# Kernel optimization log

Measured on AMD Instinct MI355X. Metric: run time of the kernel, lower is better.

The kernel has to match this reference:

```python
import jax, jax.numpy as jnp
import numpy as np

NUM_TOKENS = 8192
MODEL_DIM = 4096
NUM_EXPERTS = 64
CAPACITY_FACTOR = 1.0


def setup_inputs() -> dict:
    key = jax.random.key(0)
    k1, k2 = jax.random.split(key)
    inp = jax.random.normal(k1, (NUM_TOKENS, MODEL_DIM), dtype=jnp.float32)
    wg = jax.random.normal(k2, (NUM_EXPERTS, MODEL_DIM), dtype=jnp.float32) * (1.0 / np.sqrt(MODEL_DIM))
    return {"input": inp, "wg_weight": wg}


def reference(input, wg_weight):
    # logits = input @ wg.T  -> [T, E]
    logits = jnp.einsum('td,ed->te', input, wg_weight)
    num_tokens, num_experts = logits.shape
    capacity = int(CAPACITY_FACTOR * ((num_tokens + num_experts - 1) // num_experts))

    indices1_s = jnp.argmax(logits, axis=1)                      # [T]
    mask1 = jax.nn.one_hot(indices1_s, num_experts, dtype=logits.dtype)  # [T, E]
    gates = jax.nn.softmax(logits, axis=1)                       # [T, E]
    gates1_s = jnp.sum(gates * mask1, axis=1)                    # [T]

    # locations: position of each token within its chosen expert's queue
    # (exclusive cumsum over the one-hot mask, gathered at the chosen expert)
    locations1 = jnp.cumsum(mask1, axis=0) - 1.0                 # [T, E]
    locations1_s = jnp.sum(locations1 * mask1, axis=1).astype(jnp.int32)  # [T]

    # load-balancing aux loss (float32 branch of the original)
    me = jnp.sum(gates, axis=0)                                  # [E]
    ce = jnp.sum(mask1, axis=0)                                  # [E]
    l_aux = jnp.sum(me * ce) * (num_experts / (num_tokens * num_tokens))

    return (l_aux, indices1_s.astype(jnp.int32), locations1_s, gates1_s)
```

## Files before the change

### kernel.cpp

```cpp
#include <hip/hip_runtime.h>

namespace {
constexpr int TOK = 8192;
constexpr int DIM = 4096;
constexpr int NE  = 64;
constexpr int TB  = 128;
constexpr int KS  = 8;
constexpr int KR  = DIM / KS;
constexpr int BK  = 32;
constexpr int NT  = TOK / TB;
constexpr int NITER = KR / BK;
constexpr int LSTR = 40;
constexpr int GB  = 64;
constexpr int NCH = TOK / GB;
}

typedef _Float16 f16x8 __attribute__((ext_vector_type(8)));
typedef _Float16 f16x4 __attribute__((ext_vector_type(4)));
typedef float    f32x4 __attribute__((ext_vector_type(4)));

__global__ __launch_bounds__(256) void gemm_split(
    const float* __restrict__ A, const float* __restrict__ W,
    float* __restrict__ partial) {
  __shared__ _Float16 sm[(2 * TB + 2 * NE) * LSTR];
  _Float16* sAhi = sm;
  _Float16* sAlo = sm + TB * LSTR;
  _Float16* sWhi = sm + 2 * TB * LSTR;
  _Float16* sWlo = sm + 2 * TB * LSTR + NE * LSTR;

  const int bid  = blockIdx.x;
  const int tile = bid & (NT - 1);
  const int ks   = bid / NT;
  const int t0   = tile * TB;
  const int k0   = ks * KR;
  const int tid  = threadIdx.x;
  const int w    = tid >> 6;
  const int lane = tid & 63;
  const int col  = lane & 15;
  const int quad = lane >> 4;

  float4 ra[4], rw[2];
  {
#pragma unroll
    for (int j = 0; j < 4; ++j) {
      const int f4 = tid + 256 * j;
      const int tk = f4 >> 3, kc = (f4 & 7) * 4;
      ra[j] = *(const float4*)(A + (size_t)(t0 + tk) * DIM + k0 + kc);
    }
#pragma unroll
    for (int j = 0; j < 2; ++j) {
      const int f4 = tid + 256 * j;
      const int ee = f4 >> 3, kc = (f4 & 7) * 4;
      rw[j] = *(const float4*)(W + (size_t)ee * DIM + k0 + kc);
    }
  }

  f32x4 acc[2][4];
#pragma unroll
  for (int i = 0; i < 2; ++i)
#pragma unroll
    for (int j = 0; j < 4; ++j) acc[i][j] = (f32x4)0.0f;

  for (int it = 0; it < NITER; ++it) {
    __syncthreads();
#pragma unroll
    for (int j = 0; j < 4; ++j) {
      const int f4 = tid + 256 * j;
      const int tk = f4 >> 3, kc = (f4 & 7) * 4;
      const float4 r = ra[j];
      const _Float16 hx = (_Float16)r.x, hy = (_Float16)r.y,
                     hz = (_Float16)r.z, hw = (_Float16)r.w;
      *(f16x4*)(sAhi + tk * LSTR + kc) = (f16x4){hx, hy, hz, hw};
      *(f16x4*)(sAlo + tk * LSTR + kc) =
          (f16x4){(_Float16)(r.x - (float)hx), (_Float16)(r.y - (float)hy),
                  (_Float16)(r.z - (float)hz), (_Float16)(r.w - (float)hw)};
    }
#pragma unroll
    for (int j = 0; j < 2; ++j) {
      const int f4 = tid + 256 * j;
      const int ee = f4 >> 3, kc = (f4 & 7) * 4;
      const float4 r = rw[j];
      const _Float16 hx = (_Float16)r.x, hy = (_Float16)r.y,
                     hz = (_Float16)r.z, hw = (_Float16)r.w;
      *(f16x4*)(sWhi + ee * LSTR + kc) = (f16x4){hx, hy, hz, hw};
      *(f16x4*)(sWlo + ee * LSTR + kc) =
          (f16x4){(_Float16)(r.x - (float)hx), (_Float16)(r.y - (float)hy),
                  (_Float16)(r.z - (float)hz), (_Float16)(r.w - (float)hw)};
    }
    __syncthreads();
    if (it + 1 < NITER) {
      const int kb = k0 + (it + 1) * BK;
#pragma unroll
      for (int j = 0; j < 4; ++j) {
        const int f4 = tid + 256 * j;
        const int tk = f4 >> 3, kc = (f4 & 7) * 4;
        ra[j] = *(const float4*)(A + (size_t)(t0 + tk) * DIM + kb + kc);
      }
#pragma unroll
      for (int j = 0; j < 2; ++j) {
        const int f4 = tid + 256 * j;
        const int ee = f4 >> 3, kc = (f4 & 7) * 4;
        rw[j] = *(const float4*)(W + (size_t)ee * DIM + kb + kc);
      }
    }
    f16x8 ah[2], al[2], bh[4], bl[4];
#pragma unroll
    for (int mt = 0; mt < 2; ++mt) {
      const int r = w * 32 + mt * 16 + col;
      ah[mt] = *(const f16x8*)(sAhi + r * LSTR + quad * 8);
      al[mt] = *(const f16x8*)(sAlo + r * LSTR + quad * 8);
    }
#pragma unroll
    for (int et = 0; et < 4; ++et) {
      const int e = et * 16 + col;
      bh[et] = *(const f16x8*)(sWhi + e * LSTR + quad * 8);
      bl[et] = *(const f16x8*)(sWlo + e * LSTR + quad * 8);
    }
#pragma unroll
    for (int mt = 0; mt < 2; ++mt)
#pragma unroll
      for (int et = 0; et < 4; ++et) {
        acc[mt][et] = __builtin_amdgcn_mfma_f32_16x16x32_f16(
            ah[mt], bh[et], acc[mt][et], 0, 0, 0);
        acc[mt][et] = __builtin_amdgcn_mfma_f32_16x16x32_f16(
            ah[mt], bl[et], acc[mt][et], 0, 0, 0);
        acc[mt][et] = __builtin_amdgcn_mfma_f32_16x16x32_f16(
            al[mt], bh[et], acc[mt][et], 0, 0, 0);
      }
  }

  float* P = partial + (size_t)ks * TOK * NE;
#pragma unroll
  for (int mt = 0; mt < 2; ++mt)
#pragma unroll
    for (int et = 0; et < 4; ++et) {
      const int e = et * 16 + col;
#pragma unroll
      for (int r = 0; r < 4; ++r) {
        const int t = t0 + w * 32 + mt * 16 + quad * 4 + r;
        P[(size_t)t * NE + e] = acc[mt][et][r];
      }
    }
}

__global__ __launch_bounds__(256) void gating(
    const float* __restrict__ partial, float* __restrict__ out,
    int* __restrict__ idx_int, int* __restrict__ rankp,
    int* __restrict__ hist, float* __restrict__ me_part) {
  __shared__ float L[GB * 65];
  __shared__ float mx[GB];
  __shared__ float dninv[GB];
  __shared__ int   eid[GB];
  const int b = blockIdx.x, tid = threadIdx.x;
  const size_t base = (size_t)b * GB * NE;

#pragma unroll
  for (int j = 0; j < (GB * NE) / 256; ++j) {
    const int idx = tid + 256 * j;
    float s = 0.0f;
#pragma unroll
    for (int k = 0; k < KS; ++k)
      s += partial[(size_t)k * TOK * NE + base + idx];
    L[(idx >> 6) * 65 + (idx & 63)] = s;
  }
  __syncthreads();

  if (tid < GB) {
    const int t = tid;
    float m = -3.0e38f; int bi = 0;
    for (int e = 0; e < NE; ++e) {
      const float v = L[t * 65 + e];
      if (v > m) { m = v; bi = e; }
    }
    float s = 0.0f;
    for (int e = 0; e < NE; ++e) s += __expf(L[t * 65 + e] - m);
    const float inv = 1.0f / s;
    mx[t] = m; dninv[t] = inv; eid[t] = bi;
    const int gt = b * GB + t;
    out[1 + gt]           = (float)bi;
    out[1 + 2 * TOK + gt] = inv;
    idx_int[gt] = bi;
  }
  __syncthreads();

  if (tid < GB) {
    const int t = tid, e = eid[t];
    int r = 0;
    for (int j = 0; j < t; ++j) r += (eid[j] == e) ? 1 : 0;
    rankp[b * GB + t] = r;
    int c = 0;
    for (int t2 = 0; t2 < GB; ++t2) c += (eid[t2] == tid) ? 1 : 0;
    hist[b * NE + tid] = c;
  } else if (tid < 2 * GB) {
    const int e = tid - GB;
    float s = 0.0f;
    for (int t2 = 0; t2 < GB; ++t2)
      s += __expf(L[t2 * 65 + e] - mx[t2]) * dninv[t2];
    me_part[b * NE + e] = s;
  }
}

__global__ __launch_bounds__(256) void finalize(
    const int* __restrict__ idx_int, const int* __restrict__ rankp,
    const int* __restrict__ hist, const float* __restrict__ me_part,
    float* __restrict__ out) {
  __shared__ int   H[NCH * NE];
  __shared__ int   SEG[4 * NE];
  __shared__ float MEp[4 * NE];
  __shared__ float CE[NE];
  const int tid = threadIdx.x;
  const int e = tid & 63, seg = tid >> 6;

  for (int j = tid; j < NCH * NE; j += 256) H[j] = hist[j];
  {
    float s = 0.0f;
    for (int c = seg * 32; c < seg * 32 + 32; ++c) s += me_part[c * NE + e];
    MEp[seg * NE + e] = s;
  }
  __syncthreads();
  {
    int hs = 0;
    for (int c = seg * 32; c < seg * 32 + 32; ++c) hs += H[c * NE + e];
    SEG[seg * NE + e] = hs;
  }
  __syncthreads();
  if (tid < NE) {
    int run = 0;
    for (int s2 = 0; s2 < 4; ++s2) {
      const int v = SEG[s2 * NE + tid];
      SEG[s2 * NE + tid] = run;
      run += v;
    }
    CE[tid] = (float)run;
  }
  __syncthreads();
  {
    int run = SEG[seg * NE + e];
    for (int c = seg * 32; c < seg * 32 + 32; ++c) {
      const int v = H[c * NE + e];
      H[c * NE + e] = run;
      run += v;
    }
  }
  if (tid < 64) {
    float p = (MEp[tid] + MEp[NE + tid] + MEp[2 * NE + tid] + MEp[3 * NE + tid])
              * CE[tid];
#pragma unroll
    for (int off = 32; off > 0; off >>= 1) p += __shfl_down(p, off);
    if (tid == 0) out[0] = p * ((float)NE / ((float)TOK * (float)TOK));
  }
  __syncthreads();
#pragma unroll 4
  for (int i = tid; i < TOK; i += 256) {
    const int ex = idx_int[i];
    out[1 + TOK + i] = (float)(H[(i >> 6) * NE + ex] + rankp[i]);
  }
}

extern "C" void kernel_launch(void* const* d_in, const int* in_sizes, int n_in,
                              void* d_out, int out_size, void* d_ws, size_t ws_size,
                              hipStream_t stream) {
  const float* A = (const float*)d_in[0];
  const float* W = (const float*)d_in[1];
  float* out = (float*)d_out;
  char* ws = (char*)d_ws;

  float* partial = (float*)ws;
  const size_t poff = (size_t)KS * TOK * NE * sizeof(float);
  float* me_part = (float*)(ws + poff);
  int*  idx_int = (int*)(ws + poff + NCH * NE * sizeof(float));
  int*  rankp   = idx_int + TOK;
  int*  hist    = rankp + TOK;

  hipLaunchKernelGGL(gemm_split, dim3(NT * KS), dim3(256), 0, stream, A, W, partial);
  hipLaunchKernelGGL(gating, dim3(NCH), dim3(256), 0, stream, partial, out,
                     idx_int, rankp, hist, me_part);
  hipLaunchKernelGGL(finalize, dim3(1), dim3(256), 0, stream, idx_int, rankp,
                     hist, me_part, out);
}
```

Measured before the change: 209.6 us.

## Shrink GEMM token tile, stream A from registers, parallelize gating and finalize

The GEMM tile drops to 64 tokens per block and A fragments are loaded straight into registers in MFMA layout, so only W is split into hi/lo halves in LDS. W is double-buffered with one barrier per k-step, and launch bounds ask for higher occupancy. The gating kernel spreads max, softmax, histogram and expert-mass reductions across all 256 threads with vectorised partial loads. Finalize goes from one block to 32 blocks that each rebuild their own prefix offsets. This trades fewer barriers, less LDS traffic and more parallelism for uncoalesced-per-row A loads, twice as many GEMM blocks, and redundant histogram scans in every finalize block.

Result: no change. 209.7 us, median of 2 (+0.1%).

```diff
diff --git a/kernel.cpp b/kernel.cpp
--- a/kernel.cpp
+++ b/kernel.cpp
@@ -4,33 +4,30 @@
 constexpr int TOK = 8192;
 constexpr int DIM = 4096;
 constexpr int NE  = 64;
-constexpr int TB  = 128;
+constexpr int TB  = 64;
+constexpr int NT  = TOK / TB;
 constexpr int KS  = 8;
 constexpr int KR  = DIM / KS;
 constexpr int BK  = 32;
-constexpr int NT  = TOK / TB;
 constexpr int NITER = KR / BK;
 constexpr int LSTR = 40;
 constexpr int GB  = 64;
 constexpr int NCH = TOK / GB;
+constexpr int FB  = 32;
 }
 
 typedef _Float16 f16x8 __attribute__((ext_vector_type(8)));
 typedef _Float16 f16x4 __attribute__((ext_vector_type(4)));
 typedef float    f32x4 __attribute__((ext_vector_type(4)));
 
-__global__ __launch_bounds__(256) void gemm_split(
+__global__ __launch_bounds__(256, 4) void gemm_split(
     const float* __restrict__ A, const float* __restrict__ W,
     float* __restrict__ partial) {
-  __shared__ _Float16 sm[(2 * TB + 2 * NE) * LSTR];
-  _Float16* sAhi = sm;
-  _Float16* sAlo = sm + TB * LSTR;
-  _Float16* sWhi = sm + 2 * TB * LSTR;
-  _Float16* sWlo = sm + 2 * TB * LSTR + NE * LSTR;
+  __shared__ _Float16 sw[2][2][NE * LSTR];
 
   const int bid  = blockIdx.x;
   const int tile = bid & (NT - 1);
-  const int ks   = bid / NT;
+  const int ks   = bid >> 7;
   const int t0   = tile * TB;
   const int k0   = ks * KR;
   const int tid  = threadIdx.x;
@@ -39,108 +36,93 @@
   const int col  = lane & 15;
   const int quad = lane >> 4;
 
-  float4 ra[4], rw[2];
-  {
-#pragma unroll
-    for (int j = 0; j < 4; ++j) {
-      const int f4 = tid + 256 * j;
-      const int tk = f4 >> 3, kc = (f4 & 7) * 4;
-      ra[j] = *(const float4*)(A + (size_t)(t0 + tk) * DIM + k0 + kc);
-    }
-#pragma unroll
-    for (int j = 0; j < 2; ++j) {
-      const int f4 = tid + 256 * j;
-      const int ee = f4 >> 3, kc = (f4 & 7) * 4;
-      rw[j] = *(const float4*)(W + (size_t)ee * DIM + k0 + kc);
-    }
-  }
-
-  f32x4 acc[2][4];
-#pragma unroll
-  for (int i = 0; i < 2; ++i)
-#pragma unroll
-    for (int j = 0; j < 4; ++j) acc[i][j] = (f32x4)0.0f;
+  const float* Ap = A + (size_t)(t0 + w * 16 + col) * DIM + k0 + quad * 8;
+  const int e0  = tid >> 3,          kc0 = (tid & 7) * 4;
+  const int e1  = (tid + 256) >> 3,  kc1 = kc0;
+  const float* Wp0 = W + (size_t)e0 * DIM + k0 + kc0;
+  const float* Wp1 = W + (size_t)e1 * DIM + k0 + kc1;
+
+  float4 a0 = *(const float4*)(Ap);
+  float4 a1 = *(const float4*)(Ap + 4);
+  {
+    const float4 r0 = *(const float4*)Wp0;
+    const float4 r1 = *(const float4*)Wp1;
+    const _Float16 ax=(_Float16)r0.x, ay=(_Float16)r0.y, az=(_Float16)r0.z, aw=(_Float16)r0.w;
+    *(f16x4*)(&sw[0][0][e0*LSTR+kc0]) = (f16x4){ax,ay,az,aw};
+    *(f16x4*)(&sw[0][1][e0*LSTR+kc0]) =
+        (f16x4){(_Float16)(r0.x-(float)ax),(_Float16)(r0.y-(float)ay),
+                (_Float16)(r0.z-(float)az),(_Float16)(r0.w-(float)aw)};
+    const _Float16 bx=(_Float16)r1.x, by=(_Float16)r1.y, bz=(_Float16)r1.z, bw=(_Float16)r1.w;
+    *(f16x4*)(&sw[0][0][e1*LSTR+kc1]) = (f16x4){bx,by,bz,bw};
+    *(f16x4*)(&sw[0][1][e1*LSTR+kc1]) =
+        (f16x4){(_Float16)(r1.x-(float)bx),(_Float16)(r1.y-(float)by),
+                (_Float16)(r1.z-(float)bz),(_Float16)(r1.w-(float)bw)};
+  }
+  __syncthreads();
+
+  f32x4 acc[4];
+#pragma unroll
+  for (int j = 0; j < 4; ++j) acc[j] = (f32x4)0.0f;
 
   for (int it = 0; it < NITER; ++it) {
-    __syncthreads();
-#pragma unroll
-    for (int j = 0; j < 4; ++j) {
-      const int f4 = tid + 256 * j;
-      const int tk = f4 >> 3, kc = (f4 & 7) * 4;
-      const float4 r = ra[j];
-      const _Float16 hx = (_Float16)r.x, hy = (_Float16)r.y,
-                     hz = (_Float16)r.z, hw = (_Float16)r.w;
-      *(f16x4*)(sAhi + tk * LSTR + kc) = (f16x4){hx, hy, hz, hw};
-      *(f16x4*)(sAlo + tk * LSTR + kc) =
-          (f16x4){(_Float16)(r.x - (float)hx), (_Float16)(r.y - (float)hy),
-                  (_Float16)(r.z - (float)hz), (_Float16)(r.w - (float)hw)};
-    }
-#pragma unroll
-    for (int j = 0; j < 2; ++j) {
-      const int f4 = tid + 256 * j;
-      const int ee = f4 >> 3, kc = (f4 & 7) * 4;
-      const float4 r = rw[j];
-      const _Float16 hx = (_Float16)r.x, hy = (_Float16)r.y,
-                     hz = (_Float16)r.z, hw = (_Float16)r.w;
-      *(f16x4*)(sWhi + ee * LSTR + kc) = (f16x4){hx, hy, hz, hw};
-      *(f16x4*)(sWlo + ee * LSTR + kc) =
-          (f16x4){(_Float16)(r.x - (float)hx), (_Float16)(r.y - (float)hy),
-                  (_Float16)(r.z - (float)hz), (_Float16)(r.w - (float)hw)};
-    }
-    __syncthreads();
+    const int cur = it & 1;
+    float4 an0, an1, wn0, wn1;
     if (it + 1 < NITER) {
-      const int kb = k0 + (it + 1) * BK;
-#pragma unroll
-      for (int j = 0; j < 4; ++j) {
-        const int f4 = tid + 256 * j;
-        const int tk = f4 >> 3, kc = (f4 & 7) * 4;
-        ra[j] = *(const float4*)(A + (size_t)(t0 + tk) * DIM + kb + kc);
-      }
-#pragma unroll
-      for (int j = 0; j < 2; ++j) {
-        const int f4 = tid + 256 * j;
-        const int ee = f4 >> 3, kc = (f4 & 7) * 4;
-        rw[j] = *(const float4*)(W + (size_t)ee * DIM + kb + kc);
-      }
-    }
-    f16x8 ah[2], al[2], bh[4], bl[4];
-#pragma unroll
-    for (int mt = 0; mt < 2; ++mt) {
-      const int r = w * 32 + mt * 16 + col;
-      ah[mt] = *(const f16x8*)(sAhi + r * LSTR + quad * 8);
-      al[mt] = *(const f16x8*)(sAlo + r * LSTR + quad * 8);
-    }
+      const int kb = (it + 1) * BK;
+      an0 = *(const float4*)(Ap + kb);
+      an1 = *(const float4*)(Ap + kb + 4);
+      wn0 = *(const float4*)(Wp0 + kb);
+      wn1 = *(const float4*)(Wp1 + kb);
+    }
+    f16x8 ah, al;
+    {
+      const _Float16 h0=(_Float16)a0.x,h1=(_Float16)a0.y,h2=(_Float16)a0.z,h3=(_Float16)a0.w;
+      const _Float16 h4=(_Float16)a1.x,h5=(_Float16)a1.y,h6=(_Float16)a1.z,h7=(_Float16)a1.w;
+      ah = (f16x8){h0,h1,h2,h3,h4,h5,h6,h7};
+      al = (f16x8){(_Float16)(a0.x-(float)h0),(_Float16)(a0.y-(float)h1),
+                   (_Float16)(a0.z-(float)h2),(_Float16)(a0.w-(float)h3),
+                   (_Float16)(a1.x-(float)h4),(_Float16)(a1.y-(float)h5),
+                   (_Float16)(a1.z-(float)h6),(_Float16)(a1.w-(float)h7)};
+    }
+    f16x8 bh[4], bl[4];
 #pragma unroll
     for (int et = 0; et < 4; ++et) {
-      const int e = et * 16 + col;
-      bh[et] = *(const f16x8*)(sWhi + e * LSTR + quad * 8);
-      bl[et] = *(const f16x8*)(sWlo + e * LSTR + quad * 8);
-    }
-#pragma unroll
-    for (int mt = 0; mt < 2; ++mt)
-#pragma unroll
-      for (int et = 0; et < 4; ++et) {
-        acc[mt][et] = __builtin_amdgcn_mfma_f32_16x16x32_f16(
-            ah[mt], bh[et], acc[mt][et], 0, 0, 0);
-        acc[mt][et] = __builtin_amdgcn_mfma_f32_16x16x32_f16(
-            ah[mt], bl[et], acc[mt][et], 0, 0, 0);
-        acc[mt][et] = __builtin_amdgcn_mfma_f32_16x16x32_f16(
-            al[mt], bh[et], acc[mt][et], 0, 0, 0);
-      }
+      const int off = (et * 16 + col) * LSTR + quad * 8;
+      bh[et] = *(const f16x8*)(&sw[cur][0][off]);
+      bl[et] = *(const f16x8*)(&sw[cur][1][off]);
+    }
+#pragma unroll
+    for (int et = 0; et < 4; ++et) {
+      acc[et] = __builtin_amdgcn_mfma_f32_16x16x32_f16(ah, bh[et], acc[et], 0, 0, 0);
+      acc[et] = __builtin_amdgcn_mfma_f32_16x16x32_f16(ah, bl[et], acc[et], 0, 0, 0);
+      acc[et] = __builtin_amdgcn_mfma_f32_16x16x32_f16(al, bh[et], acc[et], 0, 0, 0);
+    }
+    if (it + 1 < NITER) {
+      const int nxt = cur ^ 1;
+      const _Float16 ax=(_Float16)wn0.x, ay=(_Float16)wn0.y, az=(_Float16)wn0.z, aw=(_Float16)wn0.w;
+      *(f16x4*)(&sw[nxt][0][e0*LSTR+kc0]) = (f16x4){ax,ay,az,aw};
+      *(f16x4*)(&sw[nxt][1][e0*LSTR+kc0]) =
+          (f16x4){(_Float16)(wn0.x-(float)ax),(_Float16)(wn0.y-(float)ay),
+                  (_Float16)(wn0.z-(float)az),(_Float16)(wn0.w-(float)aw)};
+      const _Float16 bx=(_Float16)wn1.x, by=(_Float16)wn1.y, bz=(_Float16)wn1.z, bw=(_Float16)wn1.w;
+      *(f16x4*)(&sw[nxt][0][e1*LSTR+kc1]) = (f16x4){bx,by,bz,bw};
+      *(f16x4*)(&sw[nxt][1][e1*LSTR+kc1]) =
+          (f16x4){(_Float16)(wn1.x-(float)bx),(_Float16)(wn1.y-(float)by),
+                  (_Float16)(wn1.z-(float)bz),(_Float16)(wn1.w-(float)bw)};
+      a0 = an0; a1 = an1;
+      __syncthreads();
+    }
   }
 
   float* P = partial + (size_t)ks * TOK * NE;
-#pragma unroll
-  for (int mt = 0; mt < 2; ++mt)
-#pragma unroll
-    for (int et = 0; et < 4; ++et) {
-      const int e = et * 16 + col;
-#pragma unroll
-      for (int r = 0; r < 4; ++r) {
-        const int t = t0 + w * 32 + mt * 16 + quad * 4 + r;
-        P[(size_t)t * NE + e] = acc[mt][et][r];
-      }
-    }
+  const int trow = t0 + w * 16 + quad * 4;
+#pragma unroll
+  for (int et = 0; et < 4; ++et) {
+    const int e = et * 16 + col;
+#pragma unroll
+    for (int r = 0; r < 4; ++r)
+      P[(size_t)(trow + r) * NE + e] = acc[et][r];
+  }
 }
 
 __global__ __launch_bounds__(256) void gating(
@@ -148,55 +130,86 @@
     int* __restrict__ idx_int, int* __restrict__ rankp,
     int* __restrict__ hist, float* __restrict__ me_part) {
   __shared__ float L[GB * 65];
-  __shared__ float mx[GB];
-  __shared__ float dninv[GB];
+  __shared__ float redf[4 * GB];
+  __shared__ int   redi[4 * GB];
+  __shared__ float mx[GB], dninv[GB];
   __shared__ int   eid[GB];
   const int b = blockIdx.x, tid = threadIdx.x;
-  const size_t base = (size_t)b * GB * NE;
-
-#pragma unroll
-  for (int j = 0; j < (GB * NE) / 256; ++j) {
-    const int idx = tid + 256 * j;
+  const int p = tid >> 6, l = tid & 63;
+
+  const float4* P4 = (const float4*)partial;
+  const int base4 = b * (GB * NE / 4);
+#pragma unroll
+  for (int j = 0; j < 4; ++j) {
+    const int v4 = tid + 256 * j;
+    float sx = 0.f, sy = 0.f, sz = 0.f, sww = 0.f;
+#pragma unroll
+    for (int k = 0; k < KS; ++k) {
+      const float4 v = P4[(size_t)k * (TOK * NE / 4) + base4 + v4];
+      sx += v.x; sy += v.y; sz += v.z; sww += v.w;
+    }
+    const int t = v4 >> 4, c4 = v4 & 15;
+    float* row = &L[t * 65 + c4 * 4];
+    row[0] = sx; row[1] = sy; row[2] = sz; row[3] = sww;
+  }
+  __syncthreads();
+
+  {
+    float m = -3.0e38f; int bi = 0;
+    for (int e = p * 16; e < p * 16 + 16; ++e) {
+      const float v = L[l * 65 + e];
+      if (v > m) { m = v; bi = e; }
+    }
+    redf[p * GB + l] = m; redi[p * GB + l] = bi;
+  }
+  __syncthreads();
+  if (tid < GB) {
+    float m = redf[tid]; int bi = redi[tid];
+#pragma unroll
+    for (int q = 1; q < 4; ++q) {
+      const float v = redf[q * GB + tid];
+      if (v > m) { m = v; bi = redi[q * GB + tid]; }
+    }
+    mx[tid] = m; eid[tid] = bi;
+  }
+  __syncthreads();
+
+  {
+    const float m = mx[l];
     float s = 0.0f;
-#pragma unroll
-    for (int k = 0; k < KS; ++k)
-      s += partial[(size_t)k * TOK * NE + base + idx];
-    L[(idx >> 6) * 65 + (idx & 63)] = s;
-  }
-  __syncthreads();
-
+    for (int e = p * 16; e < p * 16 + 16; ++e) {
+      const float g = __expf(L[l * 65 + e] - m);
+      L[l * 65 + e] = g; s += g;
+    }
+    redf[p * GB + l] = s;
+  }
+  __syncthreads();
   if (tid < GB) {
-    const int t = tid;
-    float m = -3.0e38f; int bi = 0;
-    for (int e = 0; e < NE; ++e) {
-      const float v = L[t * 65 + e];
-      if (v > m) { m = v; bi = e; }
-    }
-    float s = 0.0f;
-    for (int e = 0; e < NE; ++e) s += __expf(L[t * 65 + e] - m);
-    const float inv = 1.0f / s;
-    mx[t] = m; dninv[t] = inv; eid[t] = bi;
-    const int gt = b * GB + t;
-    out[1 + gt]           = (float)bi;
+    const float inv = 1.0f / (redf[tid] + redf[GB + tid] + redf[2 * GB + tid] + redf[3 * GB + tid]);
+    dninv[tid] = inv;
+    const int gt = b * GB + tid;
+    out[1 + gt]           = (float)eid[tid];
     out[1 + 2 * TOK + gt] = inv;
-    idx_int[gt] = bi;
-  }
-  __syncthreads();
-
+    idx_int[gt] = eid[tid];
+  }
+  __syncthreads();
+
+  {
+    float s = 0.0f; int c = 0;
+    for (int t2 = p * 16; t2 < p * 16 + 16; ++t2) {
+      s += L[t2 * 65 + l] * dninv[t2];
+      c += (eid[t2] == l) ? 1 : 0;
+    }
+    redf[p * GB + l] = s; redi[p * GB + l] = c;
+  }
+  __syncthreads();
   if (tid < GB) {
-    const int t = tid, e = eid[t];
+    me_part[b * NE + tid] = redf[tid] + redf[GB + tid] + redf[2 * GB + tid] + redf[3 * GB + tid];
+    hist[b * NE + tid]    = redi[tid] + redi[GB + tid] + redi[2 * GB + tid] + redi[3 * GB + tid];
+    const int e = eid[tid];
     int r = 0;
-    for (int j = 0; j < t; ++j) r += (eid[j] == e) ? 1 : 0;
-    rankp[b * GB + t] = r;
-    int c = 0;
-    for (int t2 = 0; t2 < GB; ++t2) c += (eid[t2] == tid) ? 1 : 0;
-    hist[b * NE + tid] = c;
-  } else if (tid < 2 * GB) {
-    const int e = tid - GB;
-    float s = 0.0f;
-    for (int t2 = 0; t2 < GB; ++t2)
-      s += __expf(L[t2 * 65 + e] - mx[t2]) * dninv[t2];
-    me_part[b * NE + e] = s;
+    for (int j = 0; j < tid; ++j) r += (eid[j] == e) ? 1 : 0;
+    rankp[b * GB + tid] = r;
   }
 }
 
@@ -206,17 +219,13 @@
     float* __restrict__ out) {
   __shared__ int   H[NCH * NE];
   __shared__ int   SEG[4 * NE];
-  __shared__ float MEp[4 * NE];
   __shared__ float CE[NE];
-  const int tid = threadIdx.x;
+  __shared__ int   LOC[4 * NE];
+  __shared__ float MEP[4 * NE];
+  const int b = blockIdx.x, tid = threadIdx.x;
   const int e = tid & 63, seg = tid >> 6;
 
   for (int j = tid; j < NCH * NE; j += 256) H[j] = hist[j];
-  {
-    float s = 0.0f;
-    for (int c = seg * 32; c < seg * 32 + 32; ++c) s += me_part[c * NE + e];
-    MEp[seg * NE + e] = s;
-  }
   __syncthreads();
   {
     int hs = 0;
@@ -226,6 +235,7 @@
   __syncthreads();
   if (tid < NE) {
     int run = 0;
+#pragma unroll
     for (int s2 = 0; s2 < 4; ++s2) {
       const int v = SEG[s2 * NE + tid];
       SEG[s2 * NE + tid] = run;
@@ -235,25 +245,29 @@
   }
   __syncthreads();
   {
-    int run = SEG[seg * NE + e];
-    for (int c = seg * 32; c < seg * 32 + 32; ++c) {
-      const int v = H[c * NE + e];
-      H[c * NE + e] = run;
-      run += v;
-    }
-  }
-  if (tid < 64) {
-    float p = (MEp[tid] + MEp[NE + tid] + MEp[2 * NE + tid] + MEp[3 * NE + tid])
-              * CE[tid];
-#pragma unroll
-    for (int off = 32; off > 0; off >>= 1) p += __shfl_down(p, off);
-    if (tid == 0) out[0] = p * ((float)NE / ((float)TOK * (float)TOK));
-  }
-  __syncthreads();
-#pragma unroll 4
-  for (int i = tid; i < TOK; i += 256) {
+    const int c  = 4 * b + seg;
+    const int s0 = c >> 5;
+    int run = SEG[s0 * NE + e];
+    for (int c2 = s0 * 32; c2 < c; ++c2) run += H[c2 * NE + e];
+    LOC[seg * NE + e] = run;
+  }
+  __syncthreads();
+  {
+    const int i  = b * 256 + tid;
     const int ex = idx_int[i];
-    out[1 + TOK + i] = (float)(H[(i >> 6) * NE + ex] + rankp[i]);
+    out[1 + TOK + i] = (float)(LOC[(tid >> 6) * NE + ex] + rankp[i]);
+  }
+  if (b == 0) {
+    float s = 0.0f;
+    for (int c = seg * 32; c < seg * 32 + 32; ++c) s += me_part[c * NE + e];
+    MEP[seg * NE + e] = s;
+    __syncthreads();
+    if (tid < NE) {
+      float pv = (MEP[tid] + MEP[NE + tid] + MEP[2 * NE + tid] + MEP[3 * NE + tid]) * CE[tid];
+#pragma unroll
+      for (int off = 32; off > 0; off >>= 1) pv += __shfl_down(pv, off);
+      if (tid == 0) out[0] = pv * ((float)NE / ((float)TOK * (float)TOK));
+    }
   }
 }
 
@@ -275,6 +289,6 @@
   hipLaunchKernelGGL(gemm_split, dim3(NT * KS), dim3(256), 0, stream, A, W, partial);
   hipLaunchKernelGGL(gating, dim3(NCH), dim3(256), 0, stream, partial, out,
                      idx_int, rankp, hist, me_part);
-  hipLaunchKernelGGL(finalize, dim3(1), dim3(256), 0, stream, idx_int, rankp,
+  hipLaunchKernelGGL(finalize, dim3(FB), dim3(256), 0, stream, idx_int, rankp,
                      hist, me_part, out);
 }
```

## Fuse GEMM with gating via in-block K-split and parallelize finalize

Applied to the files above, without the earlier changes.

Merges the split-K GEMM and the gating kernel into one kernel. Each 512-thread block handles 32 tokens, and its 8 waves each cover one K-slice. Operands are loaded directly from global memory into registers and split to fp16 hi/lo without an LDS staging pass. Partial sums are reduced through shared memory, removing the partial-logit round trip through global memory and one launch. Finalize now runs on 32 blocks with a per-block prefix, trading more redundant histogram loads for parallelism. The risks are uncoalesced global loads (each lane reads 32 bytes along rows) and high register pressure at 512 threads.

Result: slower. 231.7 us (+10.5%).

```diff
diff --git a/kernel.cpp b/kernel.cpp
--- a/kernel.cpp
+++ b/kernel.cpp
@@ -4,118 +4,95 @@
 constexpr int TOK = 8192;
 constexpr int DIM = 4096;
 constexpr int NE  = 64;
-constexpr int TB  = 128;
-constexpr int KS  = 8;
-constexpr int KR  = DIM / KS;
+constexpr int TB  = 32;
+constexpr int NB  = TOK / TB;
+constexpr int WK  = 8;
+constexpr int KRW = DIM / WK;
 constexpr int BK  = 32;
-constexpr int NT  = TOK / TB;
-constexpr int NITER = KR / BK;
-constexpr int LSTR = 40;
-constexpr int GB  = 64;
-constexpr int NCH = TOK / GB;
+constexpr int NITER = KRW / BK;
+constexpr int SST = 68;
+constexpr int NCH = NB;
+constexpr int FB  = 32;
 }
 
 typedef _Float16 f16x8 __attribute__((ext_vector_type(8)));
-typedef _Float16 f16x4 __attribute__((ext_vector_type(4)));
 typedef float    f32x4 __attribute__((ext_vector_type(4)));
 
-__global__ __launch_bounds__(256) void gemm_split(
+__device__ inline void cvt_split8(const float4& x, const float4& y,
+                                  f16x8& hi, f16x8& lo) {
+  const _Float16 h0 = (_Float16)x.x, h1 = (_Float16)x.y,
+                 h2 = (_Float16)x.z, h3 = (_Float16)x.w;
+  const _Float16 h4 = (_Float16)y.x, h5 = (_Float16)y.y,
+                 h6 = (_Float16)y.z, h7 = (_Float16)y.w;
+  hi = (f16x8){h0, h1, h2, h3, h4, h5, h6, h7};
+  lo = (f16x8){(_Float16)(x.x - (float)h0), (_Float16)(x.y - (float)h1),
+               (_Float16)(x.z - (float)h2), (_Float16)(x.w - (float)h3),
+               (_Float16)(y.x - (float)h4), (_Float16)(y.y - (float)h5),
+               (_Float16)(y.z - (float)h6), (_Float16)(y.w - (float)h7)};
+}
+
+__global__ __launch_bounds__(512, 2) void gemm_gate(
     const float* __restrict__ A, const float* __restrict__ W,
-    float* __restrict__ partial) {
-  __shared__ _Float16 sm[(2 * TB + 2 * NE) * LSTR];
-  _Float16* sAhi = sm;
-  _Float16* sAlo = sm + TB * LSTR;
-  _Float16* sWhi = sm + 2 * TB * LSTR;
-  _Float16* sWlo = sm + 2 * TB * LSTR + NE * LSTR;
-
-  const int bid  = blockIdx.x;
-  const int tile = bid & (NT - 1);
-  const int ks   = bid / NT;
-  const int t0   = tile * TB;
-  const int k0   = ks * KR;
+    float* __restrict__ out, int* __restrict__ idx_int,
+    int* __restrict__ rankp, int* __restrict__ hist,
+    float* __restrict__ me_part) {
+  __shared__ float slab[WK][TB * SST];
+  __shared__ float Lg[TB * NE];
+  __shared__ float redf[8 * NE];
+  __shared__ int   redi[8 * NE];
+  __shared__ float dninv[TB];
+  __shared__ int   eid[TB];
+
+  const int b    = blockIdx.x;
+  const int t0   = b * TB;
   const int tid  = threadIdx.x;
   const int w    = tid >> 6;
   const int lane = tid & 63;
   const int col  = lane & 15;
   const int quad = lane >> 4;
-
-  float4 ra[4], rw[2];
-  {
-#pragma unroll
-    for (int j = 0; j < 4; ++j) {
-      const int f4 = tid + 256 * j;
-      const int tk = f4 >> 3, kc = (f4 & 7) * 4;
-      ra[j] = *(const float4*)(A + (size_t)(t0 + tk) * DIM + k0 + kc);
-    }
-#pragma unroll
-    for (int j = 0; j < 2; ++j) {
-      const int f4 = tid + 256 * j;
-      const int ee = f4 >> 3, kc = (f4 & 7) * 4;
-      rw[j] = *(const float4*)(W + (size_t)ee * DIM + k0 + kc);
-    }
-  }
+  const int kw0  = w * KRW;
+
+  const float* Ap = A + (size_t)(t0 + col) * DIM + kw0 + quad * 8;
+  const float* Wp = W + (size_t)col * DIM + kw0 + quad * 8;
 
   f32x4 acc[2][4];
 #pragma unroll
-  for (int i = 0; i < 2; ++i)
-#pragma unroll
-    for (int j = 0; j < 4; ++j) acc[i][j] = (f32x4)0.0f;
+  for (int mt = 0; mt < 2; ++mt)
+#pragma unroll
+    for (int et = 0; et < 4; ++et) acc[mt][et] = (f32x4)0.0f;
+
+  float4 a0[2], a1[2], w0[4], w1[4];
+#pragma unroll
+  for (int mt = 0; mt < 2; ++mt) {
+    a0[mt] = *(const float4*)(Ap + (size_t)mt * 16 * DIM);
+    a1[mt] = *(const float4*)(Ap + (size_t)mt * 16 * DIM + 4);
+  }
+#pragma unroll
+  for (int et = 0; et < 4; ++et) {
+    w0[et] = *(const float4*)(Wp + (size_t)et * 16 * DIM);
+    w1[et] = *(const float4*)(Wp + (size_t)et * 16 * DIM + 4);
+  }
 
   for (int it = 0; it < NITER; ++it) {
-    __syncthreads();
-#pragma unroll
-    for (int j = 0; j < 4; ++j) {
-      const int f4 = tid + 256 * j;
-      const int tk = f4 >> 3, kc = (f4 & 7) * 4;
-      const float4 r = ra[j];
-      const _Float16 hx = (_Float16)r.x, hy = (_Float16)r.y,
-                     hz = (_Float16)r.z, hw = (_Float16)r.w;
-      *(f16x4*)(sAhi + tk * LSTR + kc) = (f16x4){hx, hy, hz, hw};
-      *(f16x4*)(sAlo + tk * LSTR + kc) =
-          (f16x4){(_Float16)(r.x - (float)hx), (_Float16)(r.y - (float)hy),
-                  (_Float16)(r.z - (float)hz), (_Float16)(r.w - (float)hw)};
-    }
-#pragma unroll
-    for (int j = 0; j < 2; ++j) {
-      const int f4 = tid + 256 * j;
-      const int ee = f4 >> 3, kc = (f4 & 7) * 4;
-      const float4 r = rw[j];
-      const _Float16 hx = (_Float16)r.x, hy = (_Float16)r.y,
-                     hz = (_Float16)r.z, hw = (_Float16)r.w;
-      *(f16x4*)(sWhi + ee * LSTR + kc) = (f16x4){hx, hy, hz, hw};
-      *(f16x4*)(sWlo + ee * LSTR + kc) =
-          (f16x4){(_Float16)(r.x - (float)hx), (_Float16)(r.y - (float)hy),
-                  (_Float16)(r.z - (float)hz), (_Float16)(r.w - (float)hw)};
-    }
-    __syncthreads();
+    float4 na0[2], na1[2], nw0[4], nw1[4];
     if (it + 1 < NITER) {
-      const int kb = k0 + (it + 1) * BK;
-#pragma unroll
-      for (int j = 0; j < 4; ++j) {
-        const int f4 = tid + 256 * j;
-        const int tk = f4 >> 3, kc = (f4 & 7) * 4;
-        ra[j] = *(const float4*)(A + (size_t)(t0 + tk) * DIM + kb + kc);
-      }
-#pragma unroll
-      for (int j = 0; j < 2; ++j) {
-        const int f4 = tid + 256 * j;
-        const int ee = f4 >> 3, kc = (f4 & 7) * 4;
-        rw[j] = *(const float4*)(W + (size_t)ee * DIM + kb + kc);
+      const int kb = (it + 1) * BK;
+#pragma unroll
+      for (int mt = 0; mt < 2; ++mt) {
+        na0[mt] = *(const float4*)(Ap + (size_t)mt * 16 * DIM + kb);
+        na1[mt] = *(const float4*)(Ap + (size_t)mt * 16 * DIM + kb + 4);
+      }
+#pragma unroll
+      for (int et = 0; et < 4; ++et) {
+        nw0[et] = *(const float4*)(Wp + (size_t)et * 16 * DIM + kb);
+        nw1[et] = *(const float4*)(Wp + (size_t)et * 16 * DIM + kb + 4);
       }
     }
     f16x8 ah[2], al[2], bh[4], bl[4];
 #pragma unroll
-    for (int mt = 0; mt < 2; ++mt) {
-      const int r = w * 32 + mt * 16 + col;
-      ah[mt] = *(const f16x8*)(sAhi + r * LSTR + quad * 8);
-      al[mt] = *(const f16x8*)(sAlo + r * LSTR + quad * 8);
-    }
-#pragma unroll
-    for (int et = 0; et < 4; ++et) {
-      const int e = et * 16 + col;
-      bh[et] = *(const f16x8*)(sWhi + e * LSTR + quad * 8);
-      bl[et] = *(const f16x8*)(sWlo + e * LSTR + quad * 8);
-    }
+    for (int mt = 0; mt < 2; ++mt) cvt_split8(a0[mt], a1[mt], ah[mt], al[mt]);
+#pragma unroll
+    for (int et = 0; et < 4; ++et) cvt_split8(w0[et], w1[et], bh[et], bl[et]);
 #pragma unroll
     for (int mt = 0; mt < 2; ++mt)
 #pragma unroll
@@ -127,9 +104,14 @@
         acc[mt][et] = __builtin_amdgcn_mfma_f32_16x16x32_f16(
             al[mt], bh[et], acc[mt][et], 0, 0, 0);
       }
-  }
-
-  float* P = partial + (size_t)ks * TOK * NE;
+    if (it + 1 < NITER) {
+#pragma unroll
+      for (int mt = 0; mt < 2; ++mt) { a0[mt] = na0[mt]; a1[mt] = na1[mt]; }
+#pragma unroll
+      for (int et = 0; et < 4; ++et) { w0[et] = nw0[et]; w1[et] = nw1[et]; }
+    }
+  }
+
 #pragma unroll
   for (int mt = 0; mt < 2; ++mt)
 #pragma unroll
@@ -137,66 +119,70 @@
       const int e = et * 16 + col;
 #pragma unroll
       for (int r = 0; r < 4; ++r) {
-        const int t = t0 + w * 32 + mt * 16 + quad * 4 + r;
-        P[(size_t)t * NE + e] = acc[mt][et][r];
-      }
-    }
-}
-
-__global__ __launch_bounds__(256) void gating(
-    const float* __restrict__ partial, float* __restrict__ out,
-    int* __restrict__ idx_int, int* __restrict__ rankp,
-    int* __restrict__ hist, float* __restrict__ me_part) {
-  __shared__ float L[GB * 65];
-  __shared__ float mx[GB];
-  __shared__ float dninv[GB];
-  __shared__ int   eid[GB];
-  const int b = blockIdx.x, tid = threadIdx.x;
-  const size_t base = (size_t)b * GB * NE;
-
-#pragma unroll
-  for (int j = 0; j < (GB * NE) / 256; ++j) {
-    const int idx = tid + 256 * j;
-    float s = 0.0f;
-#pragma unroll
-    for (int k = 0; k < KS; ++k)
-      s += partial[(size_t)k * TOK * NE + base + idx];
-    L[(idx >> 6) * 65 + (idx & 63)] = s;
-  }
-  __syncthreads();
-
-  if (tid < GB) {
-    const int t = tid;
-    float m = -3.0e38f; int bi = 0;
-    for (int e = 0; e < NE; ++e) {
-      const float v = L[t * 65 + e];
-      if (v > m) { m = v; bi = e; }
-    }
-    float s = 0.0f;
-    for (int e = 0; e < NE; ++e) s += __expf(L[t * 65 + e] - m);
+        const int tl = mt * 16 + quad * 4 + r;
+        slab[w][tl * SST + e] = acc[mt][et][r];
+      }
+    }
+  __syncthreads();
+
+  const int t   = tid >> 4;
+  const int sub = tid & 15;
+  float4 sv = (float4){0.f, 0.f, 0.f, 0.f};
+#pragma unroll
+  for (int w8 = 0; w8 < WK; ++w8) {
+    const float4 v = *(const float4*)&slab[w8][t * SST + sub * 4];
+    sv.x += v.x; sv.y += v.y; sv.z += v.z; sv.w += v.w;
+  }
+  float m = sv.x; int bi = sub * 4;
+  if (sv.y > m) { m = sv.y; bi = sub * 4 + 1; }
+  if (sv.z > m) { m = sv.z; bi = sub * 4 + 2; }
+  if (sv.w > m) { m = sv.w; bi = sub * 4 + 3; }
+#pragma unroll
+  for (int off = 8; off > 0; off >>= 1) {
+    const float ov = __shfl_xor(m, off, 16);
+    const int   oi = __shfl_xor(bi, off, 16);
+    if (ov > m || (ov == m && oi < bi)) { m = ov; bi = oi; }
+  }
+  const float g0 = __expf(sv.x - m), g1 = __expf(sv.y - m),
+              g2 = __expf(sv.z - m), g3 = __expf(sv.w - m);
+  *(float4*)&Lg[t * NE + sub * 4] = (float4){g0, g1, g2, g3};
+  float s = g0 + g1 + g2 + g3;
+#pragma unroll
+  for (int off = 8; off > 0; off >>= 1) s += __shfl_xor(s, off, 16);
+  if (sub == 0) {
     const float inv = 1.0f / s;
-    mx[t] = m; dninv[t] = inv; eid[t] = bi;
-    const int gt = b * GB + t;
+    dninv[t] = inv; eid[t] = bi;
+    const int gt = t0 + t;
     out[1 + gt]           = (float)bi;
     out[1 + 2 * TOK + gt] = inv;
     idx_int[gt] = bi;
   }
   __syncthreads();
 
-  if (tid < GB) {
-    const int t = tid, e = eid[t];
+  {
+    const int e = tid & 63, s8 = tid >> 6;
+    float ms = 0.0f; int c = 0;
+#pragma unroll
+    for (int j = 0; j < 4; ++j) {
+      const int t2 = s8 * 4 + j;
+      ms += Lg[t2 * NE + e] * dninv[t2];
+      c  += (eid[t2] == e) ? 1 : 0;
+    }
+    redf[s8 * NE + e] = ms; redi[s8 * NE + e] = c;
+  }
+  __syncthreads();
+  if (tid < NE) {
+    float ms = 0.0f; int hc = 0;
+#pragma unroll
+    for (int k = 0; k < 8; ++k) { ms += redf[k * NE + tid]; hc += redi[k * NE + tid]; }
+    me_part[b * NE + tid] = ms;
+    hist[b * NE + tid]    = hc;
+  } else if (tid < NE + TB) {
+    const int t2 = tid - NE;
+    const int ee = eid[t2];
     int r = 0;
-    for (int j = 0; j < t; ++j) r += (eid[j] == e) ? 1 : 0;
-    rankp[b * GB + t] = r;
-    int c = 0;
-    for (int t2 = 0; t2 < GB; ++t2) c += (eid[t2] == tid) ? 1 : 0;
-    hist[b * NE + tid] = c;
-  } else if (tid < 2 * GB) {
-    const int e = tid - GB;
-    float s = 0.0f;
-    for (int t2 = 0; t2 < GB; ++t2)
-      s += __expf(L[t2 * 65 + e] - mx[t2]) * dninv[t2];
-    me_part[b * NE + e] = s;
+    for (int j = 0; j < t2; ++j) r += (eid[j] == ee) ? 1 : 0;
+    rankp[t0 + t2] = r;
   }
 }
 
@@ -206,26 +192,27 @@
     float* __restrict__ out) {
   __shared__ int   H[NCH * NE];
   __shared__ int   SEG[4 * NE];
-  __shared__ float MEp[4 * NE];
   __shared__ float CE[NE];
-  const int tid = threadIdx.x;
+  __shared__ int   LOC[8 * NE];
+  __shared__ float MEP[4 * NE];
+  const int b = blockIdx.x, tid = threadIdx.x;
   const int e = tid & 63, seg = tid >> 6;
 
-  for (int j = tid; j < NCH * NE; j += 256) H[j] = hist[j];
-  {
-    float s = 0.0f;
-    for (int c = seg * 32; c < seg * 32 + 32; ++c) s += me_part[c * NE + e];
-    MEp[seg * NE + e] = s;
+  {
+    const int4* h4 = (const int4*)hist;
+    int4* H4 = (int4*)H;
+    for (int j = tid; j < NCH * NE / 4; j += 256) H4[j] = h4[j];
   }
   __syncthreads();
   {
     int hs = 0;
-    for (int c = seg * 32; c < seg * 32 + 32; ++c) hs += H[c * NE + e];
+    for (int c = seg * 64; c < seg * 64 + 64; ++c) hs += H[c * NE + e];
     SEG[seg * NE + e] = hs;
   }
   __syncthreads();
   if (tid < NE) {
     int run = 0;
+#pragma unroll
     for (int s2 = 0; s2 < 4; ++s2) {
       const int v = SEG[s2 * NE + tid];
       SEG[s2 * NE + tid] = run;
@@ -235,25 +222,31 @@
   }
   __syncthreads();
   {
-    int run = SEG[seg * NE + e];
-    for (int c = seg * 32; c < seg * 32 + 32; ++c) {
-      const int v = H[c * NE + e];
-      H[c * NE + e] = run;
-      run += v;
-    }
-  }
-  if (tid < 64) {
-    float p = (MEp[tid] + MEp[NE + tid] + MEp[2 * NE + tid] + MEp[3 * NE + tid])
-              * CE[tid];
-#pragma unroll
-    for (int off = 32; off > 0; off >>= 1) p += __shfl_down(p, off);
-    if (tid == 0) out[0] = p * ((float)NE / ((float)TOK * (float)TOK));
-  }
-  __syncthreads();
-#pragma unroll 4
-  for (int i = tid; i < TOK; i += 256) {
+    const int c  = 8 * b + seg * 2;
+    const int s0 = c >> 6;
+    int run = SEG[s0 * NE + e];
+    for (int c2 = s0 * 64; c2 < c; ++c2) run += H[c2 * NE + e];
+    LOC[(seg * 2) * NE + e]     = run;
+    LOC[(seg * 2 + 1) * NE + e] = run + H[c * NE + e];
+  }
+  __syncthreads();
+  {
+    const int i  = b * 256 + tid;
     const int ex = idx_int[i];
-    out[1 + TOK + i] = (float)(H[(i >> 6) * NE + ex] + rankp[i]);
+    out[1 + TOK + i] = (float)(LOC[(tid >> 5) * NE + ex] + rankp[i]);
+  }
+  if (b == 0) {
+    float s = 0.0f;
+    for (int c = seg * 64; c < seg * 64 + 64; ++c) s += me_part[c * NE + e];
+    MEP[seg * NE + e] = s;
+    __syncthreads();
+    if (tid < NE) {
+      float pv = (MEP[tid] + MEP[NE + tid] + MEP[2 * NE + tid] + MEP[3 * NE + tid])
+                 * CE[tid];
+#pragma unroll
+      for (int off = 32; off > 0; off >>= 1) pv += __shfl_down(pv, off);
+      if (tid == 0) out[0] = pv * ((float)NE / ((float)TOK * (float)TOK));
+    }
   }
 }
 
@@ -265,16 +258,13 @@
   float* out = (float*)d_out;
   char* ws = (char*)d_ws;
 
-  float* partial = (float*)ws;
-  const size_t poff = (size_t)KS * TOK * NE * sizeof(float);
-  float* me_part = (float*)(ws + poff);
-  int*  idx_int = (int*)(ws + poff + NCH * NE * sizeof(float));
+  float* me_part = (float*)ws;
+  int*  idx_int = (int*)(ws + (size_t)NCH * NE * sizeof(float));
   int*  rankp   = idx_int + TOK;
   int*  hist    = rankp + TOK;
 
-  hipLaunchKernelGGL(gemm_split, dim3(NT * KS), dim3(256), 0, stream, A, W, partial);
-  hipLaunchKernelGGL(gating, dim3(NCH), dim3(256), 0, stream, partial, out,
+  hipLaunchKernelGGL(gemm_gate, dim3(NB), dim3(512), 0, stream, A, W, out,
                      idx_int, rankp, hist, me_part);
-  hipLaunchKernelGGL(finalize, dim3(1), dim3(256), 0, stream, idx_int, rankp,
+  hipLaunchKernelGGL(finalize, dim3(FB), dim3(256), 0, stream, idx_int, rankp,
                      hist, me_part, out);
 }
```
